# Kernel tuning notes

Measured on AMD Instinct MI355X. Metric: run time of the kernel, lower is better.

Reference implementation:

```python
import jax, jax.numpy as jnp
import numpy as np

IN_CH = 128
EMBED = 64
ALPHA = 0.2  # leaky relu slope
NEG_INF = jnp.float32(-9e15)


def setup_inputs() -> dict:
    key = jax.random.key(0)
    k_x, k_adj, k_W, k_a, k_b = jax.random.split(key, 5)
    B, N = 2, 512
    x = jax.random.normal(k_x, (B, N, IN_CH), dtype=jnp.float32)
    adj = jax.random.randint(k_adj, (B, N, N), 0, 2, dtype=jnp.int32)
    # xavier_uniform with gain=1.414
    gain = 1.414
    lim_W = gain * np.sqrt(6.0 / (IN_CH + EMBED))
    W = jax.random.uniform(k_W, (IN_CH, EMBED), jnp.float32, -lim_W, lim_W)
    lim_a = gain * np.sqrt(6.0 / (2 * EMBED + 1))
    a = jax.random.uniform(k_a, (2 * EMBED, 1), jnp.float32, -lim_a, lim_a)
    bias = jax.random.normal(k_b, (EMBED,), dtype=jnp.float32) * 0.02
    return {"x": x, "adj": adj, "W": W, "a": a, "bias": bias}


def reference(x, adj, W, a, bias):
    B, N, _ = x.shape
    D = W.shape[1]
    hidden = jnp.matmul(x, W)                      # [B, N, D]
    # Faithful reproduction of the original's repeat_interleave/repeat + cat(dim=1) + view.
    chunks = jnp.repeat(hidden, N, axis=1)         # [B, N*N, D]
    alt = jnp.tile(hidden, (1, N, 1))              # [B, N*N, D]
    allc = jnp.concatenate([chunks, alt], axis=1).reshape(B, N, N, 2 * D)
    attn = jnp.matmul(allc, a)[..., 0]             # [B, N, N]
    attn = jnp.where(attn >= 0, attn, ALPHA * attn)  # leaky relu
    attn = jnp.where(adj > 0, attn, NEG_INF)
    attention = jax.nn.softmax(attn, axis=-1)
    # dropout omitted: reference is eval-mode (deterministic)
    out = jnp.matmul(attention, hidden) + bias     # [B, N, D]
    return out
```

## Files before the change

kernel.cpp:

```cpp
#include <hip/hip_runtime.h>
#include <math.h>

#define GN 512
#define GB 2
#define INCH 128
#define GD 64
#define ALPHA 0.2f
#define NEG_INF_F (-9e15f)
#define TI 4

__device__ __forceinline__ unsigned f2bf(float f) {
    unsigned u = __float_as_uint(f);
    return (u + 0x7FFFu + ((u >> 16) & 1u)) >> 16;
}
__device__ __forceinline__ float bf2f(unsigned short h) {
    return __uint_as_float(((unsigned)h) << 16);
}

__global__ __launch_bounds__(256) void k_hidden(
        const float* __restrict__ x, const float* __restrict__ W,
        const float* __restrict__ a,
        unsigned short* __restrict__ hbf, float* __restrict__ s1,
        float* __restrict__ s2) {
    const int row0 = blockIdx.x * 4;
    const int tid = threadIdx.x;
    __shared__ float Wl[INCH * GD];
    __shared__ float xs[4][INCH];

    const float4* W4 = (const float4*)W;
    float4* Wl4 = (float4*)Wl;
    #pragma unroll
    for (int t = 0; t < 8; ++t) Wl4[tid + t * 256] = W4[tid + t * 256];
    if (tid < 4 * INCH / 4)
        ((float4*)xs)[tid] = ((const float4*)(x + (size_t)row0 * INCH))[tid];
    __syncthreads();

    const int r = tid >> 6, d = tid & 63;
    float h = 0.f;
    #pragma unroll
    for (int k = 0; k < INCH; ++k) h = fmaf(xs[r][k], Wl[k * GD + d], h);
    hbf[(size_t)(row0 + r) * GD + d] = (unsigned short)f2bf(h);

    float p1 = a[d] * h, p2 = a[GD + d] * h;
    #pragma unroll
    for (int off = 32; off > 0; off >>= 1) {
        p1 += __shfl_xor(p1, off, 64);
        p2 += __shfl_xor(p2, off, 64);
    }
    if (d == 0) { s1[row0 + r] = p1; s2[row0 + r] = p2; }
}

__global__ __launch_bounds__(512) void k_attn(
        const int* __restrict__ adj, const unsigned short* __restrict__ hbf,
        const float* __restrict__ s1, const float* __restrict__ s2,
        const float* __restrict__ bias, float* __restrict__ out) {
    const int blk = blockIdx.x;
    const int b = blk >> 7;
    const int i0 = (blk & 127) * TI;
    const int tid = threadIdx.x;
    const int lane = tid & 63;
    const int w = tid >> 6;
    const int ld = lane & 31;
    const int lh = lane >> 5;

    __shared__ float plf[GN * TI];
    __shared__ float red[8 * TI * GD];

    const unsigned short* hbg = hbf + (size_t)b * GN * GD;
    const int j0 = w * 64;
    unsigned int hv[32];
    #pragma unroll
    for (int jj = 0; jj < 32; ++jj)
        hv[jj] = *((const unsigned int*)(hbg + (size_t)(j0 + 2 * jj + lh) * GD + 2 * ld));

    const float* s1b = s1 + b * GN;
    const float* s2b = s2 + b * GN;

    if (w < TI) {
        const int i = i0 + w;
        const int* adjw = adj + ((size_t)b * GN + i) * GN;
        float v[8];
        if (i < 256) {
            float c0 = s1b[2 * i] + s2b[2 * i];
            float c1 = s1b[2 * i + 1] + s2b[2 * i + 1];
            c0 = c0 >= 0.f ? c0 : ALPHA * c0;
            c1 = c1 >= 0.f ? c1 : ALPHA * c1;
            #pragma unroll
            for (int seg = 0; seg < 8; ++seg)
                v[seg] = adjw[seg * 64 + lane] > 0 ? (seg < 4 ? c0 : c1) : NEG_INF_F;
        } else {
            float pre4[4];
            #pragma unroll
            for (int sg = 0; sg < 4; ++sg) {
                const int m = (sg * 64 + lane) & 255;
                float pre = s1b[2 * m] + s2b[2 * m + 1];
                pre4[sg] = pre >= 0.f ? pre : ALPHA * pre;
            }
            #pragma unroll
            for (int seg = 0; seg < 8; ++seg)
                v[seg] = adjw[seg * 64 + lane] > 0 ? pre4[seg & 3] : NEG_INF_F;
        }
        float mx = v[0];
        #pragma unroll
        for (int seg = 1; seg < 8; ++seg) mx = fmaxf(mx, v[seg]);
        #pragma unroll
        for (int off = 32; off > 0; off >>= 1) mx = fmaxf(mx, __shfl_xor(mx, off, 64));
        float e[8], s = 0.f;
        #pragma unroll
        for (int seg = 0; seg < 8; ++seg) {
            e[seg] = __expf(v[seg] - mx);
            s += e[seg];
        }
        #pragma unroll
        for (int off = 32; off > 0; off >>= 1) s += __shfl_xor(s, off, 64);
        const float inv = 1.f / s;
        #pragma unroll
        for (int seg = 0; seg < 8; ++seg)
            plf[(seg * 64 + lane) * TI + w] = e[seg] * inv;
    }
    __syncthreads();

    float a00 = 0.f, a01 = 0.f, a10 = 0.f, a11 = 0.f;
    float a20 = 0.f, a21 = 0.f, a30 = 0.f, a31 = 0.f;
    #pragma unroll 8
    for (int jj = 0; jj < 32; ++jj) {
        const int j = j0 + 2 * jj + lh;
        const float4 q = *((const float4*)(plf + j * TI));
        const float h0 = bf2f((unsigned short)(hv[jj] & 0xFFFFu));
        const float h1 = bf2f((unsigned short)(hv[jj] >> 16));
        a00 = fmaf(q.x, h0, a00); a01 = fmaf(q.x, h1, a01);
        a10 = fmaf(q.y, h0, a10); a11 = fmaf(q.y, h1, a11);
        a20 = fmaf(q.z, h0, a20); a21 = fmaf(q.z, h1, a21);
        a30 = fmaf(q.w, h0, a30); a31 = fmaf(q.w, h1, a31);
    }
    a00 += __shfl_xor(a00, 32, 64); a01 += __shfl_xor(a01, 32, 64);
    a10 += __shfl_xor(a10, 32, 64); a11 += __shfl_xor(a11, 32, 64);
    a20 += __shfl_xor(a20, 32, 64); a21 += __shfl_xor(a21, 32, 64);
    a30 += __shfl_xor(a30, 32, 64); a31 += __shfl_xor(a31, 32, 64);
    if (lh == 0) {
        float2* r2 = (float2*)(red + (w * TI) * GD + 2 * ld);
        r2[0 * GD / 2]           = make_float2(a00, a01);
        *(float2*)(red + (w * TI + 1) * GD + 2 * ld) = make_float2(a10, a11);
        *(float2*)(red + (w * TI + 2) * GD + 2 * ld) = make_float2(a20, a21);
        *(float2*)(red + (w * TI + 3) * GD + 2 * ld) = make_float2(a30, a31);
    }
    __syncthreads();

    if (tid < TI * GD) {
        const int r = tid >> 6, d = tid & 63;
        float o = 0.f;
        #pragma unroll
        for (int ww = 0; ww < 8; ++ww) o += red[(ww * TI + r) * GD + d];
        o = o + bias[d];
        out[((size_t)b * GN + i0 + r) * GD + d] = o;
    }
}

extern "C" void kernel_launch(void* const* d_in, const int* in_sizes, int n_in,
                              void* d_out, int out_size, void* d_ws, size_t ws_size,
                              hipStream_t stream) {
    const float* x    = (const float*)d_in[0];
    const int*   adj  = (const int*)d_in[1];
    const float* W    = (const float*)d_in[2];
    const float* a    = (const float*)d_in[3];
    const float* bias = (const float*)d_in[4];
    float* out = (float*)d_out;

    unsigned short* hbf = (unsigned short*)d_ws;
    float* s1f = (float*)((char*)d_ws + GB * GN * GD * sizeof(unsigned short));
    float* s2f = s1f + GB * GN;

    k_hidden<<<GB * GN / 4, 256, 0, stream>>>(x, W, a, hbf, s1f, s2f);
    k_attn<<<GB * GN / TI, 512, 0, stream>>>(adj, hbf, s1f, s2f, bias, out);
}
```

Measured before the change: 14.36 us.

## Use bf16 MFMA for both projection and attention-times-hidden matmuls

Both kernels now use MFMA 16x16x32 bf16 instructions in place of scalar FMA loops. The hidden projection packs W into a swizzled bf16 LDS layout, processes 16 rows per block and stores hidden transposed. The attention kernel handles 8 rows per block with one wave per row, writes bf16 probabilities to a swizzled LDS tile and feeds them to MFMA. Precision drops further: x, W and the attention probabilities are now rounded to bf16.

```diff
diff --git a/kernel.cpp b/kernel.cpp
--- a/kernel.cpp
+++ b/kernel.cpp
@@ -7,78 +7,118 @@
 #define GD 64
 #define ALPHA 0.2f
 #define NEG_INF_F (-9e15f)
-#define TI 4
+
+typedef float f32x4 __attribute__((ext_vector_type(4)));
+typedef short short8 __attribute__((ext_vector_type(8)));
 
 __device__ __forceinline__ unsigned f2bf(float f) {
     unsigned u = __float_as_uint(f);
     return (u + 0x7FFFu + ((u >> 16) & 1u)) >> 16;
 }
-__device__ __forceinline__ float bf2f(unsigned short h) {
-    return __uint_as_float(((unsigned)h) << 16);
-}
 
 __global__ __launch_bounds__(256) void k_hidden(
         const float* __restrict__ x, const float* __restrict__ W,
         const float* __restrict__ a,
-        unsigned short* __restrict__ hbf, float* __restrict__ s1,
+        unsigned short* __restrict__ hT, float* __restrict__ s1,
         float* __restrict__ s2) {
-    const int row0 = blockIdx.x * 4;
+    const int blk = blockIdx.x;
+    const int row0 = blk * 16;
     const int tid = threadIdx.x;
-    __shared__ float Wl[INCH * GD];
-    __shared__ float xs[4][INCH];
-
-    const float4* W4 = (const float4*)W;
-    float4* Wl4 = (float4*)Wl;
-    #pragma unroll
-    for (int t = 0; t < 8; ++t) Wl4[tid + t * 256] = W4[tid + t * 256];
-    if (tid < 4 * INCH / 4)
-        ((float4*)xs)[tid] = ((const float4*)(x + (size_t)row0 * INCH))[tid];
-    __syncthreads();
-
-    const int r = tid >> 6, d = tid & 63;
-    float h = 0.f;
-    #pragma unroll
-    for (int k = 0; k < INCH; ++k) h = fmaf(xs[r][k], Wl[k * GD + d], h);
-    hbf[(size_t)(row0 + r) * GD + d] = (unsigned short)f2bf(h);
-
-    float p1 = a[d] * h, p2 = a[GD + d] * h;
-    #pragma unroll
-    for (int off = 32; off > 0; off >>= 1) {
-        p1 += __shfl_xor(p1, off, 64);
-        p2 += __shfl_xor(p2, off, 64);
-    }
-    if (d == 0) { s1[row0 + r] = p1; s2[row0 + r] = p2; }
+    const int lane = tid & 63;
+    const int w = tid >> 6;
+    const int lane15 = lane & 15;
+    const int kg = lane >> 4;
+    __shared__ char WtB[GD * 256];
+    __shared__ float sp1[4][16], sp2[4][16];
+
+    #pragma unroll
+    for (int t = 0; t < 8; ++t) {
+        const int idx = tid + t * 256;
+        const int d = idx & 63;
+        const int kq = idx >> 6;
+        unsigned short q[4];
+        #pragma unroll
+        for (int e = 0; e < 4; ++e)
+            q[e] = (unsigned short)f2bf(W[(kq * 4 + e) * GD + d]);
+        const int byte = d * 256 + (((kq >> 1) ^ (d & 7)) << 4) + (kq & 1) * 8;
+        uint2 pk;
+        pk.x = (unsigned)q[0] | ((unsigned)q[1] << 16);
+        pk.y = (unsigned)q[2] | ((unsigned)q[3] << 16);
+        *(uint2*)(WtB + byte) = pk;
+    }
+    const int dcol = w * 16 + lane15;
+    const float a1 = a[dcol], a2 = a[GD + dcol];
+    __syncthreads();
+
+    f32x4 acc = (f32x4)0.f;
+    #pragma unroll
+    for (int kt = 0; kt < 4; ++kt) {
+        const float* px = x + (size_t)(row0 + lane15) * INCH + kt * 32 + kg * 8;
+        const float4 lo = *(const float4*)px;
+        const float4 hi = *(const float4*)(px + 4);
+        int4 ai;
+        ai.x = f2bf(lo.x) | (f2bf(lo.y) << 16);
+        ai.y = f2bf(lo.z) | (f2bf(lo.w) << 16);
+        ai.z = f2bf(hi.x) | (f2bf(hi.y) << 16);
+        ai.w = f2bf(hi.z) | (f2bf(hi.w) << 16);
+        const short8 av = __builtin_bit_cast(short8, ai);
+        const short8 bv = *(const short8*)(WtB + dcol * 256 +
+                              (((kt * 4 + kg) ^ (dcol & 7)) << 4));
+        acc = __builtin_amdgcn_mfma_f32_16x16x32_bf16(av, bv, acc, 0, 0, 0);
+    }
+    uint2 hw;
+    hw.x = f2bf(acc[0]) | (f2bf(acc[1]) << 16);
+    hw.y = f2bf(acc[2]) | (f2bf(acc[3]) << 16);
+    *(uint2*)(hT + (size_t)dcol * (GB * GN) + row0 + kg * 4) = hw;
+    #pragma unroll
+    for (int r = 0; r < 4; ++r) {
+        float t1 = acc[r] * a1, t2 = acc[r] * a2;
+        #pragma unroll
+        for (int off = 1; off < 16; off <<= 1) {
+            t1 += __shfl_xor(t1, off, 64);
+            t2 += __shfl_xor(t2, off, 64);
+        }
+        if (lane15 == 0) { sp1[w][kg * 4 + r] = t1; sp2[w][kg * 4 + r] = t2; }
+    }
+    __syncthreads();
+    if (tid < 16) {
+        s1[row0 + tid] = sp1[0][tid] + sp1[1][tid] + sp1[2][tid] + sp1[3][tid];
+        s2[row0 + tid] = sp2[0][tid] + sp2[1][tid] + sp2[2][tid] + sp2[3][tid];
+    }
 }
 
 __global__ __launch_bounds__(512) void k_attn(
-        const int* __restrict__ adj, const unsigned short* __restrict__ hbf,
+        const int* __restrict__ adj, const unsigned short* __restrict__ hT,
         const float* __restrict__ s1, const float* __restrict__ s2,
         const float* __restrict__ bias, float* __restrict__ out) {
     const int blk = blockIdx.x;
-    const int b = blk >> 7;
-    const int i0 = (blk & 127) * TI;
+    const int b = blk >> 6;
+    const int i0 = (blk & 63) * 8;
     const int tid = threadIdx.x;
     const int lane = tid & 63;
     const int w = tid >> 6;
-    const int ld = lane & 31;
-    const int lh = lane >> 5;
-
-    __shared__ float plf[GN * TI];
-    __shared__ float red[8 * TI * GD];
-
-    const unsigned short* hbg = hbf + (size_t)b * GN * GD;
-    const int j0 = w * 64;
-    unsigned int hv[32];
-    #pragma unroll
-    for (int jj = 0; jj < 32; ++jj)
-        hv[jj] = *((const unsigned int*)(hbg + (size_t)(j0 + 2 * jj + lh) * GD + 2 * ld));
-
-    const float* s1b = s1 + b * GN;
-    const float* s2b = s2 + b * GN;
-
-    if (w < TI) {
+    const int lane15 = lane & 15;
+    const int kg = lane >> 4;
+
+    __shared__ unsigned short pbf[16 * GN];
+    __shared__ float red[8 * GD * 9];
+
+    short8 bv[2][4];
+    #pragma unroll
+    for (int ktl = 0; ktl < 2; ++ktl) {
+        const int kbase = w * 64 + ktl * 32;
+        #pragma unroll
+        for (int ct = 0; ct < 4; ++ct)
+            bv[ktl][ct] = *(const short8*)(hT +
+                (size_t)(ct * 16 + lane15) * (GB * GN) + b * GN + kbase + kg * 8);
+    }
+    ((uint4*)(pbf + 8 * GN))[tid] = make_uint4(0, 0, 0, 0);
+
+    {
         const int i = i0 + w;
         const int* adjw = adj + ((size_t)b * GN + i) * GN;
+        const float* s1b = s1 + b * GN;
+        const float* s2b = s2 + b * GN;
         float v[8];
         if (i < 256) {
             float c0 = s1b[2 * i] + s2b[2 * i];
@@ -115,44 +155,42 @@
         for (int off = 32; off > 0; off >>= 1) s += __shfl_xor(s, off, 64);
         const float inv = 1.f / s;
         #pragma unroll
-        for (int seg = 0; seg < 8; ++seg)
-            plf[(seg * 64 + lane) * TI + w] = e[seg] * inv;
-    }
-    __syncthreads();
-
-    float a00 = 0.f, a01 = 0.f, a10 = 0.f, a11 = 0.f;
-    float a20 = 0.f, a21 = 0.f, a30 = 0.f, a31 = 0.f;
-    #pragma unroll 8
-    for (int jj = 0; jj < 32; ++jj) {
-        const int j = j0 + 2 * jj + lh;
-        const float4 q = *((const float4*)(plf + j * TI));
-        const float h0 = bf2f((unsigned short)(hv[jj] & 0xFFFFu));
-        const float h1 = bf2f((unsigned short)(hv[jj] >> 16));
-        a00 = fmaf(q.x, h0, a00); a01 = fmaf(q.x, h1, a01);
-        a10 = fmaf(q.y, h0, a10); a11 = fmaf(q.y, h1, a11);
-        a20 = fmaf(q.z, h0, a20); a21 = fmaf(q.z, h1, a21);
-        a30 = fmaf(q.w, h0, a30); a31 = fmaf(q.w, h1, a31);
-    }
-    a00 += __shfl_xor(a00, 32, 64); a01 += __shfl_xor(a01, 32, 64);
-    a10 += __shfl_xor(a10, 32, 64); a11 += __shfl_xor(a11, 32, 64);
-    a20 += __shfl_xor(a20, 32, 64); a21 += __shfl_xor(a21, 32, 64);
-    a30 += __shfl_xor(a30, 32, 64); a31 += __shfl_xor(a31, 32, 64);
-    if (lh == 0) {
-        float2* r2 = (float2*)(red + (w * TI) * GD + 2 * ld);
-        r2[0 * GD / 2]           = make_float2(a00, a01);
-        *(float2*)(red + (w * TI + 1) * GD + 2 * ld) = make_float2(a10, a11);
-        *(float2*)(red + (w * TI + 2) * GD + 2 * ld) = make_float2(a20, a21);
-        *(float2*)(red + (w * TI + 3) * GD + 2 * ld) = make_float2(a30, a31);
-    }
-    __syncthreads();
-
-    if (tid < TI * GD) {
+        for (int seg = 0; seg < 8; ++seg) {
+            const int j = seg * 64 + lane;
+            const int byte = w * 1024 + (((j >> 3) ^ (w & 7)) << 4) + (j & 7) * 2;
+            *(unsigned short*)((char*)pbf + byte) = (unsigned short)f2bf(e[seg] * inv);
+        }
+    }
+    __syncthreads();
+
+    f32x4 acc[4];
+    #pragma unroll
+    for (int ct = 0; ct < 4; ++ct) acc[ct] = (f32x4)0.f;
+    #pragma unroll
+    for (int ktl = 0; ktl < 2; ++ktl) {
+        const int kbase = w * 64 + ktl * 32;
+        const short8 av = *(const short8*)((char*)pbf + lane15 * 1024 +
+                              ((((kbase >> 3) + kg) ^ (lane15 & 7)) << 4));
+        #pragma unroll
+        for (int ct = 0; ct < 4; ++ct)
+            acc[ct] = __builtin_amdgcn_mfma_f32_16x16x32_bf16(
+                          av, bv[ktl][ct], acc[ct], 0, 0, 0);
+    }
+    if (kg < 2) {
+        #pragma unroll
+        for (int ct = 0; ct < 4; ++ct)
+            #pragma unroll
+            for (int r = 0; r < 4; ++r)
+                red[(w * GD + ct * 16 + lane15) * 9 + kg * 4 + r] = acc[ct][r];
+    }
+    __syncthreads();
+
+    {
         const int r = tid >> 6, d = tid & 63;
         float o = 0.f;
         #pragma unroll
-        for (int ww = 0; ww < 8; ++ww) o += red[(ww * TI + r) * GD + d];
-        o = o + bias[d];
-        out[((size_t)b * GN + i0 + r) * GD + d] = o;
+        for (int ww = 0; ww < 8; ++ww) o += red[(ww * GD + d) * 9 + r];
+        out[((size_t)b * GN + i0 + r) * GD + d] = o + bias[d];
     }
 }
 
@@ -166,10 +204,10 @@
     const float* bias = (const float*)d_in[4];
     float* out = (float*)d_out;
 
-    unsigned short* hbf = (unsigned short*)d_ws;
-    float* s1f = (float*)((char*)d_ws + GB * GN * GD * sizeof(unsigned short));
+    unsigned short* hT = (unsigned short*)d_ws;
+    float* s1f = (float*)((char*)d_ws + GD * GB * GN * sizeof(unsigned short));
     float* s2f = s1f + GB * GN;
 
-    k_hidden<<<GB * GN / 4, 256, 0, stream>>>(x, W, a, hbf, s1f, s2f);
-    k_attn<<<GB * GN / TI, 512, 0, stream>>>(adj, hbf, s1f, s2f, bias, out);
-}
+    k_hidden<<<GB * GN / 16, 256, 0, stream>>>(x, W, a, hT, s1f, s2f);
+    k_attn<<<GB * GN / 8, 512, 0, stream>>>(adj, hT, s1f, s2f, bias, out);
+}
```

After: 14.74 us. +2.6%, slower.
